# Performance work log

Hardware: AMD Instinct MI355X
Metric: run time of the kernel (lower is better)

## Reference

```python
import jax, jax.numpy as jnp
import numpy as np
from math import sqrt

FACTOR = 5

def setup_inputs() -> dict:
    key = jax.random.key(0)
    kq, kk, kv, ka = jax.random.split(key, 4)
    B, L, H, D = 4, 2048, 8, 64
    return {
        "queries": jax.random.normal(kq, (B, L, H, D), dtype=jnp.float32),
        "keys": jax.random.normal(kk, (B, L, H, D), dtype=jnp.float32),
        "values": jax.random.normal(kv, (B, L, H, D), dtype=jnp.float32),
        "atten_data": jax.random.normal(ka, (B, L, 2), dtype=jnp.float32),
        "attn_mask": jnp.zeros((1,), dtype=bool),  # unused (mask_flag=False)
    }

def reference(queries, keys, values, atten_data, attn_mask):
    # layer_num=1, mask_flag=False, output_attention=False, scale=None
    B, L_Q, H, D = queries.shape
    L_K = keys.shape[1]
    U_part = min(FACTOR * int(np.ceil(np.log(L_K))), L_K)  # sample_k
    u = min(FACTOR * int(np.ceil(np.log(L_Q))), L_Q)       # n_top

    Q = jnp.transpose(queries, (0, 2, 1, 3))  # [B,H,L_Q,D]
    K = jnp.transpose(keys, (0, 2, 1, 3))     # [B,H,L_K,D]
    V = jnp.transpose(values, (0, 2, 1, 3))   # [B,H,L_V,D]

    # --- _prob_QK: random K sampling per query position ---
    index_sample = jax.random.randint(jax.random.key(42), (L_Q, U_part), 0, L_K)
    K_sample = K[:, :, index_sample, :]                      # [B,H,L_Q,U_part,D]
    Q_K_sample = jnp.einsum("bhld,bhlsd->bhls", Q, K_sample)  # [B,H,L_Q,U_part]
    M = Q_K_sample.max(axis=-1) - Q_K_sample.sum(axis=-1) / L_K  # [B,H,L_Q]
    _, M_top = jax.lax.top_k(M, u)                           # [B,H,u]

    Q_reduce = jnp.take_along_axis(Q, M_top[..., None], axis=2)  # [B,H,u,D]
    scores_top = jnp.einsum("bhud,bhkd->bhuk", Q_reduce, K)      # [B,H,u,L_K]

    scale = 1.0 / sqrt(D)
    scores_top = scores_top * scale

    # --- initial context: mean of V broadcast over L_Q (mask_flag=False) ---
    V_mean = V.mean(axis=-2, keepdims=True)                  # [B,H,1,D]
    context = jnp.broadcast_to(V_mean, (B, H, L_Q, D))

    # --- update context at top-u query positions ---
    attn = jax.nn.softmax(scores_top, axis=-1)               # [B,H,u,L_K]
    upd = jnp.einsum("bhuk,bhkd->bhud", attn, V)             # [B,H,u,D]
    bidx = jnp.arange(B)[:, None, None]
    hidx = jnp.arange(H)[None, :, None]
    context = context.at[bidx, hidx, M_top].set(upd)

    return jnp.transpose(context, (0, 2, 1, 3))  # [B,L_Q,H,D]
```

## Files before the change

kernel.cpp:

```cpp
#include <hip/hip_runtime.h>
#include <math.h>

#define B_  4
#define L_  2048
#define H_  8
#define D_  64
#define U_  40
#define HD  (H_*D_)

#define WS_NEED_KC8 2937856

struct U2 { unsigned a, b; };

__host__ __device__ constexpr unsigned rotl32c(unsigned x, int r){
  return (x<<r)|(x>>(32-r));
}

__host__ __device__ constexpr U2 tf2x32(unsigned k0, unsigned k1,
                                        unsigned x0, unsigned x1)
{
  const unsigned k2 = k0 ^ k1 ^ 0x1BD11BDAu;
  const int rA[4] = {13,15,26,6};
  const int rB[4] = {17,29,16,24};
  x0 += k0; x1 += k1;
  for (int i=0;i<4;i++){ x0+=x1; x1=rotl32c(x1,rA[i]); x1^=x0; }
  x0 += k1; x1 += k2 + 1u;
  for (int i=0;i<4;i++){ x0+=x1; x1=rotl32c(x1,rB[i]); x1^=x0; }
  x0 += k2; x1 += k0 + 2u;
  for (int i=0;i<4;i++){ x0+=x1; x1=rotl32c(x1,rA[i]); x1^=x0; }
  x0 += k0; x1 += k1 + 3u;
  for (int i=0;i<4;i++){ x0+=x1; x1=rotl32c(x1,rB[i]); x1^=x0; }
  x0 += k1; x1 += k2 + 4u;
  for (int i=0;i<4;i++){ x0+=x1; x1=rotl32c(x1,rA[i]); x1^=x0; }
  x0 += k2; x1 += k0 + 5u;
  return U2{x0, x1};
}

__global__ __launch_bounds__(256) void mvm_kernel(const float* __restrict__ q,
                                                  const float* __restrict__ k,
                                                  const float* __restrict__ v,
                                                  float* __restrict__ M,
                                                  float* __restrict__ vmean)
{
  int tid = threadIdx.x;
  int w = tid >> 6, lane = tid & 63;

  if (blockIdx.x < 512){
    int g = blockIdx.x;
    int bh = g & 31, chunk = g >> 5;
    int b = bh >> 3, h = bh & 7;
    int l0 = chunk*128 + w*32;
    float s = 0.f;
    for (int i=0;i<32;i++)
      s += v[(size_t)(b*L_ + l0 + i)*HD + h*D_ + lane];
    atomicAdd(&vmean[bh*D_ + lane], s);
    return;
  }

  int g    = blockIdx.x - 512;
  int b    = g & 3;
  int lblk = g >> 2;
  int l    = lblk*4 + w;
  int h    = lane >> 3, d8 = lane & 7;

  const float* qrow = q + (size_t)(b*L_ + l)*HD;
  float4 q0 = *(const float4*)(qrow + lane*8);
  float4 q1 = *(const float4*)(qrow + lane*8 + 4);

  constexpr U2 K2 = tf2x32(0u, 42u, 0u, 1u);
  int myidx = 0;
  if (lane < U_){
    U2 r = tf2x32(K2.a, K2.b, 0u, (unsigned)(l*U_ + lane));
    myidx = (int)((r.a ^ r.b) & 2047u);
  }

  const float* kb = k + (size_t)b*L_*HD;
  float vmax = -INFINITY, vsum = 0.f;
  #pragma unroll 8
  for (int s=0;s<U_;s++){
    int kidx = __shfl(myidx, s, 64);
    const float* kr = kb + (size_t)kidx*HD;
    float4 k0 = *(const float4*)(kr + lane*8);
    float4 k1 = *(const float4*)(kr + lane*8 + 4);
    float p = q0.x*k0.x + q0.y*k0.y + q0.z*k0.z + q0.w*k0.w
            + q1.x*k1.x + q1.y*k1.y + q1.z*k1.z + q1.w*k1.w;
    p += __shfl_xor(p, 1, 64);
    p += __shfl_xor(p, 2, 64);
    p += __shfl_xor(p, 4, 64);
    vmax = fmaxf(vmax, p);
    vsum += p;
  }
  if (d8 == 0)
    M[(b*8 + h)*L_ + l] = vmax - vsum * (1.0f/(float)L_);
}

__global__ __launch_bounds__(256) void topk_init_kernel(const float* __restrict__ M,
                                                        const float* __restrict__ vmean,
                                                        int*   __restrict__ mtop,
                                                        float* __restrict__ out)
{
  int tid = threadIdx.x;

  if (blockIdx.x >= 32){
    int i = (blockIdx.x - 32)*256 + tid;
    int d4 = i & 15;
    int h  = (i >> 4) & 7;
    int bl = i >> 7;
    int b  = bl >> 11;
    float4 vm = ((const float4*)(vmean + (b*H_ + h)*D_))[d4];
    const float sc = 1.0f/(float)L_;
    float4 o; o.x = vm.x*sc; o.y = vm.y*sc; o.z = vm.z*sc; o.w = vm.w*sc;
    ((float4*)out)[i] = o;
    return;
  }

  __shared__ unsigned keys[L_];
  __shared__ unsigned hist[256];
  __shared__ unsigned sh_prefix, sh_need, sh_cgt, sh_ceq;
  int bh = blockIdx.x;

  #pragma unroll
  for (int i=0;i<8;i++){
    unsigned bits = __float_as_uint(M[bh*L_ + tid + 256*i]);
    keys[tid + 256*i] = (bits & 0x80000000u) ? ~bits : (bits | 0x80000000u);
  }
  if (tid == 0){ sh_prefix = 0u; sh_need = U_; sh_cgt = 0u; sh_ceq = 0u; }

  unsigned pmask = 0u;
  for (int p = 3; p >= 0; --p){
    hist[tid] = 0u;
    __syncthreads();
    unsigned pref = sh_prefix;
    #pragma unroll
    for (int i=0;i<8;i++){
      unsigned key = keys[tid + 256*i];
      if ((key & pmask) == pref)
        atomicAdd(&hist[(key >> (8*p)) & 255u], 1u);
    }
    __syncthreads();

    if (tid < 64){
      unsigned h0 = hist[tid*4+0], h1 = hist[tid*4+1];
      unsigned h2 = hist[tid*4+2], h3 = hist[tid*4+3];
      unsigned loc = h0+h1+h2+h3;
      unsigned s = loc;
      #pragma unroll
      for (int off=1; off<64; off<<=1){
        unsigned o = __shfl_down(s, off, 64);
        if (tid + off < 64) s += o;
      }
      unsigned need = sh_need;
      unsigned cum = s - loc;
      unsigned bsel = 0xFFFFFFFFu, nn = 0u;
      if (cum < need && cum + h3 >= need){ bsel = tid*4+3; nn = need - cum; }
      cum += h3;
      if (bsel==0xFFFFFFFFu && cum < need && cum + h2 >= need){ bsel = tid*4+2; nn = need - cum; }
      cum += h2;
      if (bsel==0xFFFFFFFFu && cum < need && cum + h1 >= need){ bsel = tid*4+1; nn = need - cum; }
      cum += h1;
      if (bsel==0xFFFFFFFFu && cum < need && cum + h0 >= need){ bsel = tid*4+0; nn = need - cum; }
      if (bsel != 0xFFFFFFFFu){
        sh_prefix = sh_prefix | (bsel << (8*p));
        sh_need = nn;
      }
    }
    __syncthreads();
    pmask |= 0xFFu << (8*p);
  }

  unsigned K40 = sh_prefix;
  unsigned need = sh_need;
  #pragma unroll
  for (int i=0;i<8;i++){
    int idx = tid + 256*i;
    unsigned key = keys[idx];
    if (key > K40){
      unsigned pos = atomicAdd(&sh_cgt, 1u);
      mtop[bh*U_ + pos] = idx;
    } else if (key == K40){
      unsigned e = atomicAdd(&sh_ceq, 1u);
      if (e < need) mtop[bh*U_ + (U_ - need) + e] = idx;
    }
  }
}

__global__ __launch_bounds__(256, 3) void attn_kernel(const float* __restrict__ q,
                                                      const float* __restrict__ k,
                                                      const float* __restrict__ v,
                                                      const int*   __restrict__ mtop,
                                                      float* __restrict__ pacc,
                                                      float* __restrict__ pl,
                                                      int nt, int KC)
{
  __shared__ float sh[128*68 + 128*64 + 20*64];
  float* Kt  = sh;
  float* Vt  = sh + 128*68;
  float* Qs  = sh + 128*68 + 128*64;
  float* psQ = sh;

  int g  = blockIdx.x;
  int bh = g & 31, j = g >> 5;
  int kc = j >> 1, qg = j & 1;
  int b = bh >> 3, h = bh & 7;
  int tid = threadIdx.x, w = tid >> 6, lane = tid & 63;

  #pragma unroll
  for (int c=0;c<2;c++){
    int flat = c*256 + tid;
    if (flat < 320){
      int row = flat >> 4, col = flat & 15;
      int lstar = mtop[bh*U_ + qg*20 + row];
      ((float4*)(Qs + row*64))[col] =
        ((const float4*)(q + (size_t)(b*L_ + lstar)*HD + h*D_))[col];
    }
  }

  float acc[5], lsum[5];
  #pragma unroll
  for (int qq=0;qq<5;qq++){ acc[qq] = 0.f; lsum[qq] = 0.f; }

  for (int tt=0; tt<nt; ++tt){
    int kt = (kc*nt + tt)*128;
    __syncthreads();
    #pragma unroll
    for (int c=0;c<8;c++){
      int flat = c*256 + tid;
      int row = flat >> 4, col = flat & 15;
      ((float4*)(Kt + row*68))[col] =
        ((const float4*)(k + (size_t)(b*L_ + kt + row)*HD + h*D_))[col];
      ((float4*)(Vt + row*64))[col] =
        ((const float4*)(v + (size_t)(b*L_ + kt + row)*HD + h*D_))[col];
    }
    __syncthreads();

    float s0[5], s1[5];
    #pragma unroll
    for (int qq=0;qq<5;qq++){ s0[qq] = 0.f; s1[qq] = 0.f; }
    const float* kr0 = Kt + lane*68;
    const float* kr1 = Kt + (lane+64)*68;
    #pragma unroll
    for (int t=0;t<16;t++){
      float4 k0 = ((const float4*)kr0)[t];
      float4 k1 = ((const float4*)kr1)[t];
      #pragma unroll
      for (int qq=0;qq<5;qq++){
        float4 qf = ((const float4*)(Qs + (w*5+qq)*64))[t];
        s0[qq] += k0.x*qf.x + k0.y*qf.y + k0.z*qf.z + k0.w*qf.w;
        s1[qq] += k1.x*qf.x + k1.y*qf.y + k1.z*qf.z + k1.w*qf.w;
      }
    }
    __syncthreads();

    #pragma unroll
    for (int qq=0;qq<5;qq++){
      float p0 = __expf(s0[qq]*0.125f);
      float p1 = __expf(s1[qq]*0.125f);
      psQ[(w*5+qq)*128 + lane]      = p0;
      psQ[(w*5+qq)*128 + lane + 64] = p1;
      lsum[qq] += p0 + p1;
    }
    __syncthreads();

    for (int k4=0;k4<32;k4++){
      float v0 = Vt[(4*k4+0)*64 + lane];
      float v1 = Vt[(4*k4+1)*64 + lane];
      float v2 = Vt[(4*k4+2)*64 + lane];
      float v3 = Vt[(4*k4+3)*64 + lane];
      #pragma unroll
      for (int qq=0;qq<5;qq++){
        float4 pp = ((const float4*)(psQ + (w*5+qq)*128))[k4];
        acc[qq] += pp.x*v0 + pp.y*v1 + pp.z*v2 + pp.w*v3;
      }
    }
  }

  #pragma unroll
  for (int qq=0;qq<5;qq++){
    float ls = lsum[qq];
    #pragma unroll
    for (int off=32; off; off>>=1) ls += __shfl_xor(ls, off, 64);
    int gu = bh*U_ + qg*20 + w*5 + qq;
    pacc[(size_t)(gu*KC + kc)*64 + lane] = acc[qq];
    if (lane == 0) pl[gu*KC + kc] = ls;
  }
}

__global__ __launch_bounds__(256) void combine_kernel(const int* __restrict__ mtop,
                                                      const float* __restrict__ pacc,
                                                      const float* __restrict__ pl,
                                                      float* __restrict__ out,
                                                      int KC)
{
  int gu = blockIdx.x*4 + (threadIdx.x >> 6);
  int lane = threadIdx.x & 63;
  int bh = gu / U_, u = gu - bh*U_;
  float a = 0.f, L = 0.f;
  for (int c=0;c<KC;c++){
    a += pacc[(size_t)(gu*KC + c)*64 + lane];
    L += pl[gu*KC + c];
  }
  int b = bh >> 3, h = bh & 7;
  int lstar = mtop[bh*U_ + u];
  out[(size_t)(b*L_ + lstar)*HD + h*D_ + lane] = a / L;
}

extern "C" void kernel_launch(void* const* d_in, const int* in_sizes, int n_in,
                              void* d_out, int out_size, void* d_ws, size_t ws_size,
                              hipStream_t stream)
{
  const float* q = (const float*)d_in[0];
  const float* k = (const float*)d_in[1];
  const float* v = (const float*)d_in[2];
  float* out = (float*)d_out;

  int KC = (ws_size >= (size_t)WS_NEED_KC8) ? 8 : 4;
  int nt = 16 / KC;

  size_t o_pl    = (size_t)1280*KC*64*4;
  size_t o_vmean = o_pl + (size_t)1280*KC*4;
  size_t o_M     = o_vmean + 2048*4;
  size_t o_mtop  = o_M + 65536*4;

  float* pacc  = (float*)d_ws;
  float* pl    = (float*)((char*)d_ws + o_pl);
  float* vmean = (float*)((char*)d_ws + o_vmean);
  float* M     = (float*)((char*)d_ws + o_M);
  int*   mtop  = (int*)  ((char*)d_ws + o_mtop);

  hipMemsetAsync(vmean, 0, 2048*sizeof(float), stream);
  mvm_kernel      <<<2560,  256, 0, stream>>>(q, k, v, M, vmean);
  topk_init_kernel<<<4128,  256, 0, stream>>>(M, vmean, mtop, out);
  attn_kernel     <<<64*KC, 256, 0, stream>>>(q, k, v, mtop, pacc, pl, nt, KC);
  combine_kernel  <<<320,   256, 0, stream>>>(mtop, pacc, pl, out, KC);
}
```

Before: 157.0 us.

## Process all 40 top queries per block and read V straight from global

```diff
diff --git a/kernel.cpp b/kernel.cpp
--- a/kernel.cpp
+++ b/kernel.cpp
@@ -8,7 +8,8 @@
 #define U_  40
 #define HD  (H_*D_)
 
-#define WS_NEED_KC8 2937856
+#define WS_NEED_KC16 5600256
+#define WS_NEED_KC8  2937856
 
 struct U2 { unsigned a, b; };
 
@@ -192,50 +193,46 @@
                                                       float* __restrict__ pl,
                                                       int nt, int KC)
 {
-  __shared__ float sh[128*68 + 128*64 + 20*64];
+  __shared__ float sh[128*68 + 40*64];
   float* Kt  = sh;
-  float* Vt  = sh + 128*68;
-  float* Qs  = sh + 128*68 + 128*64;
+  float* Qs  = sh + 128*68;
   float* psQ = sh;
 
   int g  = blockIdx.x;
-  int bh = g & 31, j = g >> 5;
-  int kc = j >> 1, qg = j & 1;
+  int bh = g & 31, kc = g >> 5;
   int b = bh >> 3, h = bh & 7;
   int tid = threadIdx.x, w = tid >> 6, lane = tid & 63;
 
   #pragma unroll
-  for (int c=0;c<2;c++){
+  for (int c=0;c<3;c++){
     int flat = c*256 + tid;
-    if (flat < 320){
+    if (flat < 640){
       int row = flat >> 4, col = flat & 15;
-      int lstar = mtop[bh*U_ + qg*20 + row];
+      int lstar = mtop[bh*U_ + row];
       ((float4*)(Qs + row*64))[col] =
         ((const float4*)(q + (size_t)(b*L_ + lstar)*HD + h*D_))[col];
     }
   }
 
-  float acc[5], lsum[5];
-  #pragma unroll
-  for (int qq=0;qq<5;qq++){ acc[qq] = 0.f; lsum[qq] = 0.f; }
+  float acc[10], lsum[10];
+  #pragma unroll
+  for (int qq=0;qq<10;qq++){ acc[qq] = 0.f; lsum[qq] = 0.f; }
 
   for (int tt=0; tt<nt; ++tt){
     int kt = (kc*nt + tt)*128;
-    __syncthreads();
+    if (tt) __syncthreads();
     #pragma unroll
     for (int c=0;c<8;c++){
       int flat = c*256 + tid;
       int row = flat >> 4, col = flat & 15;
       ((float4*)(Kt + row*68))[col] =
         ((const float4*)(k + (size_t)(b*L_ + kt + row)*HD + h*D_))[col];
-      ((float4*)(Vt + row*64))[col] =
-        ((const float4*)(v + (size_t)(b*L_ + kt + row)*HD + h*D_))[col];
-    }
-    __syncthreads();
-
-    float s0[5], s1[5];
-    #pragma unroll
-    for (int qq=0;qq<5;qq++){ s0[qq] = 0.f; s1[qq] = 0.f; }
+    }
+    __syncthreads();
+
+    float s0[10], s1[10];
+    #pragma unroll
+    for (int qq=0;qq<10;qq++){ s0[qq] = 0.f; s1[qq] = 0.f; }
     const float* kr0 = Kt + lane*68;
     const float* kr1 = Kt + (lane+64)*68;
     #pragma unroll
@@ -243,8 +240,8 @@
       float4 k0 = ((const float4*)kr0)[t];
       float4 k1 = ((const float4*)kr1)[t];
       #pragma unroll
-      for (int qq=0;qq<5;qq++){
-        float4 qf = ((const float4*)(Qs + (w*5+qq)*64))[t];
+      for (int qq=0;qq<10;qq++){
+        float4 qf = ((const float4*)(Qs + (w*10+qq)*64))[t];
         s0[qq] += k0.x*qf.x + k0.y*qf.y + k0.z*qf.z + k0.w*qf.w;
         s1[qq] += k1.x*qf.x + k1.y*qf.y + k1.z*qf.z + k1.w*qf.w;
       }
@@ -252,34 +249,35 @@
     __syncthreads();
 
     #pragma unroll
-    for (int qq=0;qq<5;qq++){
+    for (int qq=0;qq<10;qq++){
       float p0 = __expf(s0[qq]*0.125f);
       float p1 = __expf(s1[qq]*0.125f);
-      psQ[(w*5+qq)*128 + lane]      = p0;
-      psQ[(w*5+qq)*128 + lane + 64] = p1;
+      psQ[(w*10+qq)*128 + lane]      = p0;
+      psQ[(w*10+qq)*128 + lane + 64] = p1;
       lsum[qq] += p0 + p1;
     }
-    __syncthreads();
-
+
+    const float* vb = v + (size_t)(b*L_ + kt)*HD + h*D_ + lane;
+    #pragma unroll 4
     for (int k4=0;k4<32;k4++){
-      float v0 = Vt[(4*k4+0)*64 + lane];
-      float v1 = Vt[(4*k4+1)*64 + lane];
-      float v2 = Vt[(4*k4+2)*64 + lane];
-      float v3 = Vt[(4*k4+3)*64 + lane];
+      float v0 = vb[(size_t)(4*k4+0)*HD];
+      float v1 = vb[(size_t)(4*k4+1)*HD];
+      float v2 = vb[(size_t)(4*k4+2)*HD];
+      float v3 = vb[(size_t)(4*k4+3)*HD];
       #pragma unroll
-      for (int qq=0;qq<5;qq++){
-        float4 pp = ((const float4*)(psQ + (w*5+qq)*128))[k4];
+      for (int qq=0;qq<10;qq++){
+        float4 pp = ((const float4*)(psQ + (w*10+qq)*128))[k4];
         acc[qq] += pp.x*v0 + pp.y*v1 + pp.z*v2 + pp.w*v3;
       }
     }
   }
 
   #pragma unroll
-  for (int qq=0;qq<5;qq++){
+  for (int qq=0;qq<10;qq++){
     float ls = lsum[qq];
     #pragma unroll
     for (int off=32; off; off>>=1) ls += __shfl_xor(ls, off, 64);
-    int gu = bh*U_ + qg*20 + w*5 + qq;
+    int gu = bh*U_ + w*10 + qq;
     pacc[(size_t)(gu*KC + kc)*64 + lane] = acc[qq];
     if (lane == 0) pl[gu*KC + kc] = ls;
   }
@@ -313,7 +311,7 @@
   const float* v = (const float*)d_in[2];
   float* out = (float*)d_out;
 
-  int KC = (ws_size >= (size_t)WS_NEED_KC8) ? 8 : 4;
+  int KC = (ws_size >= (size_t)WS_NEED_KC16) ? 16 : 8;
   int nt = 16 / KC;
 
   size_t o_pl    = (size_t)1280*KC*64*4;
@@ -330,6 +328,6 @@
   hipMemsetAsync(vmean, 0, 2048*sizeof(float), stream);
   mvm_kernel      <<<2560,  256, 0, stream>>>(q, k, v, M, vmean);
   topk_init_kernel<<<4128,  256, 0, stream>>>(M, vmean, mtop, out);
-  attn_kernel     <<<64*KC, 256, 0, stream>>>(q, k, v, mtop, pacc, pl, nt, KC);
+  attn_kernel     <<<32*KC, 256, 0, stream>>>(q, k, v, mtop, pacc, pl, nt, KC);
   combine_kernel  <<<320,   256, 0, stream>>>(mtop, pacc, pl, out, KC);
 }
```

After: 173.0 us. +10.2%, slower.

## Remove attention barriers via per-wave P buffer and reduce V mean without atomics

Applied to the files above, without the earlier changes.

```diff
diff --git a/kernel.cpp b/kernel.cpp
--- a/kernel.cpp
+++ b/kernel.cpp
@@ -45,19 +45,23 @@
   int tid = threadIdx.x;
   int w = tid >> 6, lane = tid & 63;
 
-  if (blockIdx.x < 512){
-    int g = blockIdx.x;
-    int bh = g & 31, chunk = g >> 5;
+  if (blockIdx.x < 32){
+    __shared__ float red[4][64];
+    int bh = blockIdx.x;
     int b = bh >> 3, h = bh & 7;
-    int l0 = chunk*128 + w*32;
+    const float* vb = v + (size_t)b*L_*HD + h*D_ + lane;
+    int l0 = w*512;
     float s = 0.f;
-    for (int i=0;i<32;i++)
-      s += v[(size_t)(b*L_ + l0 + i)*HD + h*D_ + lane];
-    atomicAdd(&vmean[bh*D_ + lane], s);
+    for (int i=0;i<512;i++)
+      s += vb[(size_t)(l0 + i)*HD];
+    red[w][lane] = s;
+    __syncthreads();
+    if (w == 0)
+      vmean[bh*D_ + lane] = red[0][lane]+red[1][lane]+red[2][lane]+red[3][lane];
     return;
   }
 
-  int g    = blockIdx.x - 512;
+  int g    = blockIdx.x - 32;
   int b    = g & 3;
   int lblk = g >> 2;
   int l    = lblk*4 + w;
@@ -192,11 +196,11 @@
                                                       float* __restrict__ pl,
                                                       int nt, int KC)
 {
-  __shared__ float sh[128*68 + 128*64 + 20*64];
+  __shared__ float sh[128*68 + 128*64 + 20*64 + 20*64];
   float* Kt  = sh;
   float* Vt  = sh + 128*68;
   float* Qs  = sh + 128*68 + 128*64;
-  float* psQ = sh;
+  float* psQ = Qs + 20*64;
 
   int g  = blockIdx.x;
   int bh = g & 31, j = g >> 5;
@@ -221,7 +225,7 @@
 
   for (int tt=0; tt<nt; ++tt){
     int kt = (kc*nt + tt)*128;
-    __syncthreads();
+    if (tt) __syncthreads();
     #pragma unroll
     for (int c=0;c<8;c++){
       int flat = c*256 + tid;
@@ -249,27 +253,27 @@
         s1[qq] += k1.x*qf.x + k1.y*qf.y + k1.z*qf.z + k1.w*qf.w;
       }
     }
-    __syncthreads();
-
-    #pragma unroll
-    for (int qq=0;qq<5;qq++){
-      float p0 = __expf(s0[qq]*0.125f);
-      float p1 = __expf(s1[qq]*0.125f);
-      psQ[(w*5+qq)*128 + lane]      = p0;
-      psQ[(w*5+qq)*128 + lane + 64] = p1;
-      lsum[qq] += p0 + p1;
-    }
-    __syncthreads();
-
-    for (int k4=0;k4<32;k4++){
-      float v0 = Vt[(4*k4+0)*64 + lane];
-      float v1 = Vt[(4*k4+1)*64 + lane];
-      float v2 = Vt[(4*k4+2)*64 + lane];
-      float v3 = Vt[(4*k4+3)*64 + lane];
+
+    #pragma unroll
+    for (int half=0; half<2; ++half){
       #pragma unroll
       for (int qq=0;qq<5;qq++){
-        float4 pp = ((const float4*)(psQ + (w*5+qq)*128))[k4];
-        acc[qq] += pp.x*v0 + pp.y*v1 + pp.z*v2 + pp.w*v3;
+        float p = __expf((half ? s1[qq] : s0[qq])*0.125f);
+        psQ[(w*5+qq)*64 + lane] = p;
+        lsum[qq] += p;
+      }
+      #pragma unroll 4
+      for (int k4=0;k4<16;k4++){
+        int rb = half*64 + k4*4;
+        float v0 = Vt[(rb+0)*64 + lane];
+        float v1 = Vt[(rb+1)*64 + lane];
+        float v2 = Vt[(rb+2)*64 + lane];
+        float v3 = Vt[(rb+3)*64 + lane];
+        #pragma unroll
+        for (int qq=0;qq<5;qq++){
+          float4 pp = ((const float4*)(psQ + (w*5+qq)*64))[k4];
+          acc[qq] += pp.x*v0 + pp.y*v1 + pp.z*v2 + pp.w*v3;
+        }
       }
     }
   }
@@ -327,8 +331,7 @@
   float* M     = (float*)((char*)d_ws + o_M);
   int*   mtop  = (int*)  ((char*)d_ws + o_mtop);
 
-  hipMemsetAsync(vmean, 0, 2048*sizeof(float), stream);
-  mvm_kernel      <<<2560,  256, 0, stream>>>(q, k, v, M, vmean);
+  mvm_kernel      <<<2080,  256, 0, stream>>>(q, k, v, M, vmean);
   topk_init_kernel<<<4128,  256, 0, stream>>>(M, vmean, mtop, out);
   attn_kernel     <<<64*KC, 256, 0, stream>>>(q, k, v, mtop, pacc, pl, nt, KC);
   combine_kernel  <<<320,   256, 0, stream>>>(mtop, pacc, pl, out, KC);
```

Result: slower. 172.4 us (+9.8%).
